# Kernel tuning notes

Measured on AMD Instinct MI355X. Metric: run time of the kernel, lower is better.

## Reference

```python
import jax, jax.numpy as jnp
import numpy as np

N_NODES = 100000
N_EDGES = 50000
D = 128        # node feature dim
NNZ = 1600000  # number of (node, hyperedge) incidence pairs


def setup_inputs() -> dict:
    key = jax.random.key(0)
    k1, k2, k3, k4, k5 = jax.random.split(key, 5)
    y = jax.random.normal(k1, (N_NODES * D,), dtype=jnp.float32)
    node_idx = jax.random.randint(k2, (NNZ,), 0, N_NODES, dtype=jnp.int32)
    edge_idx = jax.random.randint(k3, (NNZ,), 0, N_EDGES, dtype=jnp.int32)
    incidence = jnp.stack([node_idx, edge_idx])  # [2, NNZ]
    scale = jnp.float32(1.0 / np.sqrt(D))
    W1 = jax.random.normal(k4, (D, D), dtype=jnp.float32) * scale
    W2 = jax.random.normal(k5, (D, D), dtype=jnp.float32) * scale
    b1 = jnp.zeros((D,), dtype=jnp.float32)
    b2 = jnp.zeros((D,), dtype=jnp.float32)
    return {"t": jnp.float32(0.0), "y": y, "incidence": incidence,
            "W1": W1, "b1": b1, "W2": W2, "b2": b2}


def reference(t, y, incidence, W1, b1, W2, b2):
    # reshape flat SDE state to (n, d) -- the wrapper's core job
    X = y.reshape(N_NODES, D)
    n_idx = incidence[0]
    e_idx = incidence[1]
    ones = jnp.ones((NNZ,), dtype=X.dtype)

    # node -> hyperedge: linear map, gather by node, mean-aggregate per edge
    msg = X @ W1 + b1                                   # [n, d]
    edge_sum = jax.ops.segment_sum(msg[n_idx], e_idx, num_segments=N_EDGES)
    edge_deg = jax.ops.segment_sum(ones, e_idx, num_segments=N_EDGES)
    edge_feat = edge_sum / jnp.maximum(edge_deg, 1.0)[:, None]  # [e, d]

    # hyperedge -> node: linear map, gather by edge, mean-aggregate per node
    out_msg = edge_feat @ W2 + b2                       # [e, d]
    node_sum = jax.ops.segment_sum(out_msg[e_idx], n_idx, num_segments=N_NODES)
    node_deg = jax.ops.segment_sum(ones, n_idx, num_segments=N_NODES)
    x_new = node_sum / jnp.maximum(node_deg, 1.0)[:, None]      # [n, d]

    # activation + flatten back to 1D drift
    return jax.nn.relu(x_new).reshape(-1)
```

## Files before the change

kernel.cpp:

```cpp
#include <hip/hip_runtime.h>

#define NN_NODES 100000
#define NN_EDGES 50000
#define DD 128
#define NNZP 1600000
#define NT_SEG (NN_EDGES + NN_NODES)
#define TOTP (2 * NNZP)
#define BKT_SHIFT 9
#define NBKT ((NT_SEG + 511) / 512)
#define TILE 8192
#define NBIN ((TOTP + TILE - 1) / TILE)
#define CVTBLK 1024
#define SMAX 18432
#define CAP 20480
#define VMASK 0xFFFFF

typedef unsigned int uint;
typedef unsigned short ushort;
typedef __attribute__((ext_vector_type(8))) short bf16x8;
typedef __attribute__((ext_vector_type(4))) float f32x4;

__device__ __forceinline__ float bf_lo(uint u) {
  union { uint i; float f; } c; c.i = u << 16; return c.f;
}
__device__ __forceinline__ float bf_hi(uint u) {
  union { uint i; float f; } c; c.i = u & 0xffff0000u; return c.f;
}
__device__ __forceinline__ ushort f2bf(float f) {
  union { float f; uint i; } c; c.f = f;
  uint r = c.i + 0x7fffu + ((c.i >> 16) & 1u);
  return (ushort)(r >> 16);
}

__device__ __forceinline__ void block_excl_scan_512(const int* __restrict__ arr,
                                                    int* __restrict__ out,
                                                    int* __restrict__ wsum) {
  int t = threadIdx.x;
  int v = arr[t];
  int lane = t & 63, wid = t >> 6;
  int s = v;
  #pragma unroll
  for (int o = 1; o < 64; o <<= 1) {
    int u = __shfl_up(s, o, 64);
    if (lane >= o) s += u;
  }
  if (lane == 63) wsum[wid] = s;
  __syncthreads();
  int add = 0;
  for (int w = 0; w < wid; ++w) add += wsum[w];
  out[t] = s + add - v;
}

__global__ __launch_bounds__(512) void k_bin(const int* __restrict__ ninc,
                                             const int* __restrict__ einc,
                                             int* __restrict__ bktcur,
                                             int* __restrict__ pbuf,
                                             const float* __restrict__ X,
                                             ushort* __restrict__ Xb,
                                             const float* __restrict__ W1,
                                             const float* __restrict__ W2,
                                             const float* __restrict__ b1,
                                             const float* __restrict__ b2,
                                             ushort* __restrict__ Wct,
                                             float* __restrict__ bc) {
  __shared__ int spack[TILE];
  __shared__ ushort sbkt[TILE];
  __shared__ int bhist[512], bexcl[512], bcur[512], brun[512], wsum[8];
  const int b = blockIdx.x;
  const int t = threadIdx.x;
  if (b >= NBIN + CVTBLK) {
    const int bb = b - NBIN - CVTBLK;
    float* sW1 = (float*)spack;
    for (int i = t; i < 8 * 32; i += 512)
      reinterpret_cast<float4*>(sW1)[i] = reinterpret_cast<const float4*>(W1 + bb * 8 * DD)[i];
    __syncthreads();
    if (t < 256) {
      const int lr = t >> 5;
      const int cg = t & 31;
      float s0 = 0.f, s1 = 0.f, s2 = 0.f, s3 = 0.f;
      for (int j = 0; j < DD; ++j) {
        float a = sW1[lr * DD + j];
        float4 w = reinterpret_cast<const float4*>(W2)[j * 32 + cg];
        s0 += a * w.x; s1 += a * w.y; s2 += a * w.z; s3 += a * w.w;
      }
      const int grow = bb * 8 + lr;
      const int c0 = cg * 4;
      Wct[(size_t)(c0 + 0) * DD + grow] = f2bf(s0);
      Wct[(size_t)(c0 + 1) * DD + grow] = f2bf(s1);
      Wct[(size_t)(c0 + 2) * DD + grow] = f2bf(s2);
      Wct[(size_t)(c0 + 3) * DD + grow] = f2bf(s3);
    }
    if (bb == 0 && t >= 256 && t < 256 + DD) {
      int c = t - 256;
      float s = b2[c];
      for (int j = 0; j < DD; ++j) s += b1[j] * W2[(size_t)j * DD + c];
      bc[c] = s;
    }
    return;
  }
  if (b >= NBIN) {
    const int stride = CVTBLK * 512;
    for (int i = (b - NBIN) * 512 + t; i < NN_NODES * DD / 4; i += stride) {
      float4 v = reinterpret_cast<const float4*>(X)[i];
      ushort4 o;
      o.x = f2bf(v.x); o.y = f2bf(v.y); o.z = f2bf(v.z); o.w = f2bf(v.w);
      reinterpret_cast<ushort4*>(Xb)[i] = o;
    }
    return;
  }
  const int i0 = b * TILE;
  const int V = min(TILE, TOTP - i0);
  int pseg[16], pval[16];
  bhist[t] = 0;
  __syncthreads();
  #pragma unroll
  for (int j = 0; j < 16; ++j) {
    int e = t + j * 512;
    if (e < V) {
      int i = i0 + e;
      int seg, val;
      if (i < NNZP) { seg = einc[i]; val = ninc[i]; }
      else          { seg = NN_EDGES + ninc[i - NNZP]; val = einc[i - NNZP]; }
      pseg[j] = seg; pval[j] = val;
      atomicAdd(&bhist[seg >> BKT_SHIFT], 1);
    }
  }
  __syncthreads();
  block_excl_scan_512(bhist, bexcl, wsum);
  __syncthreads();
  if (t < NBKT && bhist[t] > 0)
    brun[t] = t * CAP + atomicAdd(&bktcur[t], bhist[t]);
  bcur[t] = bexcl[t];
  __syncthreads();
  #pragma unroll
  for (int j = 0; j < 16; ++j) {
    int e = t + j * 512;
    if (e < V) {
      int bk = pseg[j] >> BKT_SHIFT;
      int slot = atomicAdd(&bcur[bk], 1);
      spack[slot] = ((pseg[j] & 511) << 20) | pval[j];
      sbkt[slot] = (ushort)bk;
    }
  }
  __syncthreads();
  for (int e = t; e < V; e += 512) {
    int bk = sbkt[e];
    int gpos = brun[bk] + (e - bexcl[bk]);
    if (gpos < (bk + 1) * CAP)
      pbuf[gpos] = spack[e];
  }
}

__global__ __launch_bounds__(512) void k_place(const int* __restrict__ bktcnt,
                                               const int* __restrict__ pbuf,
                                               int* __restrict__ offs,
                                               int* __restrict__ list) {
  __shared__ int shist[512], sexcl[512], scur[512], wsum[8], red[8];
  __shared__ int stage[SMAX];
  const int b = blockIdx.x;
  const int t = threadIdx.x;
  int part = 0;
  for (int i = t; i < b; i += 512) part += min(bktcnt[i], CAP);
  #pragma unroll
  for (int o = 1; o < 64; o <<= 1) part += __shfl_xor(part, o, 64);
  if ((t & 63) == 0) red[t >> 6] = part;
  shist[t] = 0;
  __syncthreads();
  int base = 0;
  #pragma unroll
  for (int w = 0; w < 8; ++w) base += red[w];
  const int sb = b * CAP;
  const int s = min(bktcnt[b], CAP);
  for (int e = t; e < s; e += 512) atomicAdd(&shist[pbuf[sb + e] >> 20], 1);
  __syncthreads();
  block_excl_scan_512(shist, sexcl, wsum);
  __syncthreads();
  int seg = (b << BKT_SHIFT) + t;
  if (seg < NT_SEG) offs[seg] = base + sexcl[t];
  if (b == 0 && t == 0) offs[NT_SEG] = TOTP;
  scur[t] = sexcl[t];
  __syncthreads();
  if (s <= SMAX) {
    for (int e = t; e < s; e += 512) {
      int p = pbuf[sb + e];
      int slot = atomicAdd(&scur[p >> 20], 1);
      stage[slot] = p & VMASK;
    }
    __syncthreads();
    for (int e = t; e < s; e += 512) list[base + e] = stage[e];
  } else {
    for (int e = t; e < s; e += 512) {
      int p = pbuf[sb + e];
      int r = atomicAdd(&scur[p >> 20], 1);
      list[base + r] = p & VMASK;
    }
  }
}

#define ACC8(V) do { \
    acc[0] += bf_lo(V.x); acc[1] += bf_hi(V.x); \
    acc[2] += bf_lo(V.y); acc[3] += bf_hi(V.y); \
    acc[4] += bf_lo(V.z); acc[5] += bf_hi(V.z); \
    acc[6] += bf_lo(V.w); acc[7] += bf_hi(V.w); } while (0)

template<int MODE>
__global__ __launch_bounds__(256) void k_agg(const ushort* __restrict__ src,
                                             void* __restrict__ dstv,
                                             const float* __restrict__ bias,
                                             const int* __restrict__ offs,
                                             const int* __restrict__ list,
                                             int nseg, int segbase) {
  int g = (int)((blockIdx.x * blockDim.x + threadIdx.x) >> 4);
  int t = threadIdx.x & 15;
  if (g >= nseg) return;
  int b0 = offs[segbase + g];
  int deg = offs[segbase + g + 1] - b0;
  float acc[8];
  #pragma unroll
  for (int j = 0; j < 8; ++j) acc[j] = 0.f;
  const int* lp = list + b0;
  int ida[8];
  #pragma unroll
  for (int j = 0; j < 8; ++j) ida[j] = lp[j];
  int chunk = 0;
  while (chunk + 8 <= deg) {
    uint4 vb[8];
    #pragma unroll
    for (int j = 0; j < 8; ++j)
      vb[j] = reinterpret_cast<const uint4*>(src + (size_t)ida[j] * DD)[t];
    int idb[8];
    #pragma unroll
    for (int j = 0; j < 8; ++j) idb[j] = lp[chunk + 8 + j];
    #pragma unroll
    for (int j = 0; j < 8; ++j) ACC8(vb[j]);
    #pragma unroll
    for (int j = 0; j < 8; ++j) ida[j] = idb[j];
    chunk += 8;
  }
  if (chunk < deg) {
    uint4 vb[8];
    #pragma unroll
    for (int j = 0; j < 8; ++j) {
      uint4 v = make_uint4(0u, 0u, 0u, 0u);
      if (chunk + j < deg)
        v = reinterpret_cast<const uint4*>(src + (size_t)ida[j] * DD)[t];
      vb[j] = v;
    }
    #pragma unroll
    for (int j = 0; j < 8; ++j) ACC8(vb[j]);
  }
  float inv = 1.0f / fmaxf((float)deg, 1.0f);
  if (MODE == 0) {
    ushort* dst = (ushort*)dstv;
    uint4 o;
    o.x = (uint)f2bf(acc[0] * inv) | ((uint)f2bf(acc[1] * inv) << 16);
    o.y = (uint)f2bf(acc[2] * inv) | ((uint)f2bf(acc[3] * inv) << 16);
    o.z = (uint)f2bf(acc[4] * inv) | ((uint)f2bf(acc[5] * inv) << 16);
    o.w = (uint)f2bf(acc[6] * inv) | ((uint)f2bf(acc[7] * inv) << 16);
    reinterpret_cast<uint4*>(dst + (size_t)g * DD)[t] = o;
  } else {
    float flag = (deg > 0) ? 1.f : 0.f;
    float4 bb0 = reinterpret_cast<const float4*>(bias)[2 * t];
    float4 bb1 = reinterpret_cast<const float4*>(bias)[2 * t + 1];
    float4 o0, o1;
    o0.x = fmaxf(acc[0] * inv + bb0.x * flag, 0.f);
    o0.y = fmaxf(acc[1] * inv + bb0.y * flag, 0.f);
    o0.z = fmaxf(acc[2] * inv + bb0.z * flag, 0.f);
    o0.w = fmaxf(acc[3] * inv + bb0.w * flag, 0.f);
    o1.x = fmaxf(acc[4] * inv + bb1.x * flag, 0.f);
    o1.y = fmaxf(acc[5] * inv + bb1.y * flag, 0.f);
    o1.z = fmaxf(acc[6] * inv + bb1.z * flag, 0.f);
    o1.w = fmaxf(acc[7] * inv + bb1.w * flag, 0.f);
    float* orow = (float*)dstv + (size_t)g * DD;
    reinterpret_cast<float4*>(orow)[2 * t] = o0;
    reinterpret_cast<float4*>(orow)[2 * t + 1] = o1;
  }
}

__global__ __launch_bounds__(256) void k_gemm_mfma(
    const ushort* __restrict__ A, ushort* __restrict__ C,
    const ushort* __restrict__ Wt, int M) {
  __shared__ ushort sA[DD * DD];
  __shared__ ushort sW[DD * DD];
  const int tid = threadIdx.x;
  const int R = blockIdx.x * DD;
  const int rows = min(DD, M - R);
  for (int i = tid; i < DD * 16; i += 256) {
    int r = i >> 4, c8 = i & 15;
    uint4 v = reinterpret_cast<const uint4*>(Wt + (size_t)r * DD)[c8];
    int bo = (c8 * 16) ^ ((r & 7) << 4);
    *reinterpret_cast<uint4*>(reinterpret_cast<char*>(sW) + r * 256 + bo) = v;
  }
  for (int i = tid; i < DD * 16; i += 256) {
    int r = i >> 4, c8 = i & 15;
    uint4 v = make_uint4(0u, 0u, 0u, 0u);
    if (r < rows) v = reinterpret_cast<const uint4*>(A + (size_t)(R + r) * DD)[c8];
    int bo = (c8 * 16) ^ ((r & 7) << 4);
    *reinterpret_cast<uint4*>(reinterpret_cast<char*>(sA) + r * 256 + bo) = v;
  }
  __syncthreads();
  const int wid = tid >> 6;
  const int l = tid & 63;
  const int lr = l & 15;
  const int lg = l >> 4;
  const int wrow = wid * 32;
  f32x4 acc[2][8];
  #pragma unroll
  for (int a = 0; a < 2; ++a)
    #pragma unroll
    for (int b = 0; b < 8; ++b) acc[a][b] = (f32x4){0.f, 0.f, 0.f, 0.f};
  const char* cA = reinterpret_cast<const char*>(sA);
  const char* cW = reinterpret_cast<const char*>(sW);
  #pragma unroll
  for (int k0 = 0; k0 < 4; ++k0) {
    int kb = k0 * 64 + lg * 16;
    int r0 = wrow + lr, r1 = wrow + 16 + lr;
    bf16x8 a0 = *reinterpret_cast<const bf16x8*>(cA + r0 * 256 + (kb ^ ((r0 & 7) << 4)));
    bf16x8 a1 = *reinterpret_cast<const bf16x8*>(cA + r1 * 256 + (kb ^ ((r1 & 7) << 4)));
    bf16x8 bfr[8];
    #pragma unroll
    for (int ct = 0; ct < 8; ++ct) {
      int c = ct * 16 + lr;
      bfr[ct] = *reinterpret_cast<const bf16x8*>(cW + c * 256 + (kb ^ ((c & 7) << 4)));
    }
    #pragma unroll
    for (int ct = 0; ct < 8; ++ct) {
      acc[0][ct] = __builtin_amdgcn_mfma_f32_16x16x32_bf16(a0, bfr[ct], acc[0][ct], 0, 0, 0);
      acc[1][ct] = __builtin_amdgcn_mfma_f32_16x16x32_bf16(a1, bfr[ct], acc[1][ct], 0, 0, 0);
    }
  }
  #pragma unroll
  for (int rt = 0; rt < 2; ++rt) {
    #pragma unroll
    for (int j = 0; j < 4; ++j) {
      int r = wrow + rt * 16 + lg * 4 + j;
      if (r < rows) {
        int gr = R + r;
        #pragma unroll
        for (int ct = 0; ct < 8; ++ct)
          C[(size_t)gr * DD + ct * 16 + lr] = f2bf(acc[rt][ct][j]);
      }
    }
  }
}

extern "C" void kernel_launch(void* const* d_in, const int* in_sizes, int n_in,
                              void* d_out, int out_size, void* d_ws, size_t ws_size,
                              hipStream_t stream) {
  const float* X   = (const float*)d_in[1];
  const int*   inc = (const int*)d_in[2];
  const float* W1  = (const float*)d_in[3];
  const float* b1  = (const float*)d_in[4];
  const float* W2  = (const float*)d_in[5];
  const float* b2  = (const float*)d_in[6];
  float* out = (float*)d_out;
  const int* ninc = inc;
  const int* einc = inc + NNZP;

  char* wsp = (char*)d_ws;
  int* pbuf    = (int*)wsp;    wsp += (size_t)NBKT * CAP * sizeof(int);
  ushort* Xb   = (ushort*)wsp; wsp += (size_t)NN_NODES * DD * sizeof(ushort);
  int* offs    = (int*)wsp;    wsp += (size_t)(NT_SEG + 1) * sizeof(int);
  int* list    = (int*)wsp;    wsp += (size_t)TOTP * sizeof(int);
  int* bktcur  = (int*)wsp;    wsp += 512 * sizeof(int);
  ushort* Wct  = (ushort*)wsp; wsp += (size_t)DD * DD * sizeof(ushort);
  float* bc    = (float*)wsp;  wsp += DD * sizeof(float);
  ushort* bufE = (ushort*)pbuf;

  hipMemsetAsync(bktcur, 0, 512 * sizeof(int), stream);

  k_bin<<<NBIN + CVTBLK + 16, 512, 0, stream>>>(ninc, einc, bktcur, pbuf,
                                                X, Xb, W1, W2, b1, b2, Wct, bc);
  k_place<<<NBKT, 512, 0, stream>>>(bktcur, pbuf, offs, list);

  k_agg<0><<<(NN_EDGES * 16 + 255) / 256, 256, 0, stream>>>(Xb, bufE, nullptr, offs, list, NN_EDGES, 0);
  k_gemm_mfma<<<(NN_EDGES + DD - 1) / DD, 256, 0, stream>>>(bufE, bufE, Wct, NN_EDGES);
  k_agg<1><<<(NN_NODES * 16 + 255) / 256, 256, 0, stream>>>(bufE, out, bc, offs, list, NN_NODES, NN_EDGES);
}
```

Before: 173.8 us.

## Sort segments by degree descending to balance aggregation load across waves

Builds a per-region degree histogram in k_place, scans it, and scatters segment ids into a permutation ordered by descending degree. The aggregation kernels then process segments through this permutation, so groups of similar degree run together and heavy segments start early, reducing tail imbalance. The cost is two extra kernel launches, extra memory traffic for perm, and scattered output writes. Degrees here are near-Poisson (mean 32 and 16), so the imbalance being removed is modest.

```diff
diff --git a/kernel.cpp b/kernel.cpp
--- a/kernel.cpp
+++ b/kernel.cpp
@@ -154,7 +154,8 @@
 __global__ __launch_bounds__(512) void k_place(const int* __restrict__ bktcnt,
                                                const int* __restrict__ pbuf,
                                                int* __restrict__ offs,
-                                               int* __restrict__ list) {
+                                               int* __restrict__ list,
+                                               int* __restrict__ dhist) {
   __shared__ int shist[512], sexcl[512], scur[512], wsum[8], red[8];
   __shared__ int stage[SMAX];
   const int b = blockIdx.x;
@@ -173,6 +174,14 @@
   const int s = min(bktcnt[b], CAP);
   for (int e = t; e < s; e += 512) atomicAdd(&shist[pbuf[sb + e] >> 20], 1);
   __syncthreads();
+  {
+    int segg = (b << BKT_SHIFT) + t;
+    if (segg < NT_SEG) {
+      int region = (segg < NN_EDGES) ? 0 : 1;
+      int bin = region * 256 + (255 - min(shist[t], 255));
+      atomicAdd(&dhist[bin], 1);
+    }
+  }
   block_excl_scan_512(shist, sexcl, wsum);
   __syncthreads();
   int seg = (b << BKT_SHIFT) + t;
@@ -197,6 +206,41 @@
   }
 }
 
+__global__ void k_dscan(const int* __restrict__ dhist, int* __restrict__ dcur) {
+  __shared__ int arr[512], out[512], wsum[8];
+  int t = threadIdx.x;
+  arr[t] = dhist[t];
+  __syncthreads();
+  block_excl_scan_512(arr, out, wsum);
+  __syncthreads();
+  dcur[t] = out[t];
+}
+
+__global__ __launch_bounds__(512) void k_dscat(const int* __restrict__ offs,
+                                               int* __restrict__ dcur,
+                                               int* __restrict__ perm) {
+  __shared__ int bhist[512], brun[512], bcur[512];
+  const int t = threadIdx.x;
+  const int i = blockIdx.x * 512 + t;
+  bhist[t] = 0; bcur[t] = 0;
+  __syncthreads();
+  int bin = 0;
+  const bool valid = (i < NT_SEG);
+  if (valid) {
+    int dg = offs[i + 1] - offs[i];
+    int region = (i < NN_EDGES) ? 0 : 1;
+    bin = region * 256 + (255 - min(dg, 255));
+    atomicAdd(&bhist[bin], 1);
+  }
+  __syncthreads();
+  if (bhist[t] > 0) brun[t] = atomicAdd(&dcur[t], bhist[t]);
+  __syncthreads();
+  if (valid) {
+    int r = atomicAdd(&bcur[bin], 1);
+    perm[brun[bin] + r] = (i < NN_EDGES) ? i : i - NN_EDGES;
+  }
+}
+
 #define ACC8(V) do { \
     acc[0] += bf_lo(V.x); acc[1] += bf_hi(V.x); \
     acc[2] += bf_lo(V.y); acc[3] += bf_hi(V.y); \
@@ -209,12 +253,14 @@
                                              const float* __restrict__ bias,
                                              const int* __restrict__ offs,
                                              const int* __restrict__ list,
+                                             const int* __restrict__ perm,
                                              int nseg, int segbase) {
   int g = (int)((blockIdx.x * blockDim.x + threadIdx.x) >> 4);
   int t = threadIdx.x & 15;
   if (g >= nseg) return;
-  int b0 = offs[segbase + g];
-  int deg = offs[segbase + g + 1] - b0;
+  int p = perm[segbase + g];
+  int b0 = offs[segbase + p];
+  int deg = offs[segbase + p + 1] - b0;
   float acc[8];
   #pragma unroll
   for (int j = 0; j < 8; ++j) acc[j] = 0.f;
@@ -257,7 +303,7 @@
     o.y = (uint)f2bf(acc[2] * inv) | ((uint)f2bf(acc[3] * inv) << 16);
     o.z = (uint)f2bf(acc[4] * inv) | ((uint)f2bf(acc[5] * inv) << 16);
     o.w = (uint)f2bf(acc[6] * inv) | ((uint)f2bf(acc[7] * inv) << 16);
-    reinterpret_cast<uint4*>(dst + (size_t)g * DD)[t] = o;
+    reinterpret_cast<uint4*>(dst + (size_t)p * DD)[t] = o;
   } else {
     float flag = (deg > 0) ? 1.f : 0.f;
     float4 bb0 = reinterpret_cast<const float4*>(bias)[2 * t];
@@ -271,7 +317,7 @@
     o1.y = fmaxf(acc[5] * inv + bb1.y * flag, 0.f);
     o1.z = fmaxf(acc[6] * inv + bb1.z * flag, 0.f);
     o1.w = fmaxf(acc[7] * inv + bb1.w * flag, 0.f);
-    float* orow = (float*)dstv + (size_t)g * DD;
+    float* orow = (float*)dstv + (size_t)p * DD;
     reinterpret_cast<float4*>(orow)[2 * t] = o0;
     reinterpret_cast<float4*>(orow)[2 * t + 1] = o1;
   }
@@ -362,18 +408,23 @@
   ushort* Xb   = (ushort*)wsp; wsp += (size_t)NN_NODES * DD * sizeof(ushort);
   int* offs    = (int*)wsp;    wsp += (size_t)(NT_SEG + 1) * sizeof(int);
   int* list    = (int*)wsp;    wsp += (size_t)TOTP * sizeof(int);
+  int* perm    = (int*)wsp;    wsp += (size_t)NT_SEG * sizeof(int);
   int* bktcur  = (int*)wsp;    wsp += 512 * sizeof(int);
+  int* dhist   = (int*)wsp;    wsp += 512 * sizeof(int);
+  int* dcur    = (int*)wsp;    wsp += 512 * sizeof(int);
   ushort* Wct  = (ushort*)wsp; wsp += (size_t)DD * DD * sizeof(ushort);
   float* bc    = (float*)wsp;  wsp += DD * sizeof(float);
   ushort* bufE = (ushort*)pbuf;
 
-  hipMemsetAsync(bktcur, 0, 512 * sizeof(int), stream);
+  hipMemsetAsync(bktcur, 0, 1024 * sizeof(int), stream);
 
   k_bin<<<NBIN + CVTBLK + 16, 512, 0, stream>>>(ninc, einc, bktcur, pbuf,
                                                 X, Xb, W1, W2, b1, b2, Wct, bc);
-  k_place<<<NBKT, 512, 0, stream>>>(bktcur, pbuf, offs, list);
-
-  k_agg<0><<<(NN_EDGES * 16 + 255) / 256, 256, 0, stream>>>(Xb, bufE, nullptr, offs, list, NN_EDGES, 0);
+  k_place<<<NBKT, 512, 0, stream>>>(bktcur, pbuf, offs, list, dhist);
+  k_dscan<<<1, 512, 0, stream>>>(dhist, dcur);
+  k_dscat<<<(NT_SEG + 511) / 512, 512, 0, stream>>>(offs, dcur, perm);
+
+  k_agg<0><<<(NN_EDGES * 16 + 255) / 256, 256, 0, stream>>>(Xb, bufE, nullptr, offs, list, perm, NN_EDGES, 0);
   k_gemm_mfma<<<(NN_EDGES + DD - 1) / DD, 256, 0, stream>>>(bufE, bufE, Wct, NN_EDGES);
-  k_agg<1><<<(NN_NODES * 16 + 255) / 256, 256, 0, stream>>>(bufE, out, bc, offs, list, NN_NODES, NN_EDGES);
-}
+  k_agg<1><<<(NN_NODES * 16 + 255) / 256, 256, 0, stream>>>(bufE, out, bc, offs, list, perm, NN_NODES, NN_EDGES);
+}
```

New measurement: 453.4 us. +160.9%, slower.
